# Kernel tuning notes

Measured on AMD Instinct MI355X. Metric: run time of the kernel, lower is better.

The kernel has to match this reference:

```python
import jax, jax.numpy as jnp
import numpy as np

B, K, DIN, D, NH, HD, FF = 16384, 64, 49, 16, 2, 8, 32
EPS = 1e-5


def _ln(x, g, b):
    m = jnp.mean(x, axis=-1, keepdims=True)
    v = jnp.mean((x - m) ** 2, axis=-1, keepdims=True)
    return (x - m) / jnp.sqrt(v + EPS) * g + b


def setup_inputs() -> dict:
    key = jax.random.key(0)
    ks = jax.random.split(key, 20)
    s = 0.05
    return {
        "x": jax.random.normal(ks[0], (B, K, DIN), dtype=jnp.float32),
        # torch Linear layout: weight is [out, in]
        "proj_w": jax.random.normal(ks[1], (D, DIN), dtype=jnp.float32) * s,
        "proj_b": jax.random.normal(ks[2], (D,), dtype=jnp.float32) * s,
        "pos": jax.random.normal(ks[3], (1, K, D), dtype=jnp.float32) * s,
        "in_proj_w": jax.random.normal(ks[4], (3 * D, D), dtype=jnp.float32) * s,
        "in_proj_b": jax.random.normal(ks[5], (3 * D,), dtype=jnp.float32) * s,
        "out_w": jax.random.normal(ks[6], (D, D), dtype=jnp.float32) * s,
        "out_b": jax.random.normal(ks[7], (D,), dtype=jnp.float32) * s,
        "ln1_g": jnp.ones((D,), dtype=jnp.float32),
        "ln1_b": jnp.zeros((D,), dtype=jnp.float32),
        "lin1_w": jax.random.normal(ks[8], (FF, D), dtype=jnp.float32) * s,
        "lin1_b": jax.random.normal(ks[9], (FF,), dtype=jnp.float32) * s,
        "lin2_w": jax.random.normal(ks[10], (D, FF), dtype=jnp.float32) * s,
        "lin2_b": jax.random.normal(ks[11], (D,), dtype=jnp.float32) * s,
        "ln2_g": jnp.ones((D,), dtype=jnp.float32),
        "ln2_b": jnp.zeros((D,), dtype=jnp.float32),
        "head_w": jax.random.normal(ks[12], (1, D), dtype=jnp.float32) * s,
        "head_b": jax.random.normal(ks[13], (1,), dtype=jnp.float32) * s,
    }


def reference(x, proj_w, proj_b, pos, in_proj_w, in_proj_b, out_w, out_b,
              ln1_g, ln1_b, lin1_w, lin1_b, lin2_w, lin2_b, ln2_g, ln2_b,
              head_w, head_b):
    # input projection + learned positional embedding
    h = jnp.einsum("bki,di->bkd", x, proj_w) + proj_b + pos  # [B,K,D]

    # --- self-attention (torch MultiheadAttention, post-norm encoder layer) ---
    qkv = jnp.einsum("bkd,ed->bke", h, in_proj_w) + in_proj_b  # [B,K,3D]
    q, k, v = jnp.split(qkv, 3, axis=-1)
    q = q.reshape(B, K, NH, HD)
    k = k.reshape(B, K, NH, HD)
    v = v.reshape(B, K, NH, HD)
    scores = jnp.einsum("bqhd,bkhd->bhqk", q, k) / jnp.sqrt(jnp.float32(HD))
    attn = jax.nn.softmax(scores, axis=-1)
    ctx = jnp.einsum("bhqk,bkhd->bqhd", attn, v).reshape(B, K, D)
    attn_out = jnp.einsum("bkd,od->bko", ctx, out_w) + out_b
    h = _ln(h + attn_out, ln1_g, ln1_b)

    # --- FFN (relu), post-norm ---
    ff = jnp.einsum("bkd,fd->bkf", h, lin1_w) + lin1_b
    ff = jax.nn.relu(ff)
    ff = jnp.einsum("bkf,df->bkd", ff, lin2_w) + lin2_b
    h = _ln(h + ff, ln2_g, ln2_b)

    # mean pool over sequence, then scalar head
    pooled = h.mean(axis=1)  # [B,D]
    out = jnp.einsum("bd,od->bo", pooled, head_w) + head_b
    return out.squeeze(-1)  # [B]
```

## Files before the change

### kernel.cpp

```cpp
#include <hip/hip_runtime.h>


#define SCALE 0.510069729f

#define KRS   40
#define VTB   2560
#define VTS   72
#define PRB   3712
#define PRS   72
#define HRB   8320
#define HRS   40
#define RED   10880
#define SMTOT 10888

#define WS_HB   2304
#define WS_EP   3328

typedef __bf16 v8bf __attribute__((ext_vector_type(8)));
typedef float  v4f  __attribute__((ext_vector_type(4)));

#define LDS_ORDER() __asm__ volatile("" ::: "memory")

static __device__ __forceinline__ short f2bs(float f) {
    __bf16 h = (__bf16)f;
    return __builtin_bit_cast(short, h);
}
#define MFMA(a,b,c) __builtin_amdgcn_mfma_f32_16x16x32_bf16((a),(b),(c),0,0,0)

template<int IMM> static __device__ __forceinline__ float swz(float x) {
    return __builtin_bit_cast(float,
        __builtin_amdgcn_ds_swizzle(__builtin_bit_cast(int, x), IMM));
}

static __device__ __forceinline__ void red16(v4f& v) {
    #pragma unroll
    for (int r = 0; r < 4; ++r) v[r] += swz<0x041F>(v[r]);
    #pragma unroll
    for (int r = 0; r < 4; ++r) v[r] += swz<0x081F>(v[r]);
    #pragma unroll
    for (int r = 0; r < 4; ++r) v[r] += swz<0x101F>(v[r]);
    #pragma unroll
    for (int r = 0; r < 4; ++r) v[r] += swz<0x201F>(v[r]);
}

__global__ __launch_bounds__(64)
void tx_prep(const float* __restrict__ proj_w, const float* __restrict__ proj_b,
             const float* __restrict__ pos,
             const float* __restrict__ in_proj_w, const float* __restrict__ in_proj_b,
             const float* __restrict__ out_w, const float* __restrict__ out_b,
             const float* __restrict__ ln1_g, const float* __restrict__ ln1_b,
             const float* __restrict__ lin1_w, const float* __restrict__ lin1_b,
             const float* __restrict__ lin2_w, const float* __restrict__ lin2_b,
             const float* __restrict__ ln2_g, const float* __restrict__ ln2_b,
             const float* __restrict__ head_w, float* __restrict__ ws)
{
    const int lane = threadIdx.x, g = lane >> 4, c = lane & 15;
    v8bf* wf = (v8bf*)ws;
    v8bf F;
    #pragma unroll
    for (int j = 0; j < 8; ++j) F[j] = (__bf16)proj_w[c*49 + g*8 + j];
    wf[0*64 + lane] = F;
    #pragma unroll
    for (int j = 0; j < 8; ++j) { int k = 32 + g*8 + j; F[j] = (k < 49) ? (__bf16)proj_w[c*49 + k] : (__bf16)0.f; }
    wf[1*64 + lane] = F;
    #pragma unroll
    for (int nt = 0; nt < 3; ++nt) {
        #pragma unroll
        for (int j = 0; j < 8; ++j) { int k = g*8 + j; F[j] = (k < 16) ? (__bf16)in_proj_w[(nt*16 + c)*16 + k] : (__bf16)0.f; }
        wf[(2 + nt)*64 + lane] = F;
    }
    #pragma unroll
    for (int j = 0; j < 8; ++j) { int k = g*8 + j; F[j] = (k < 16) ? (__bf16)out_w[c*16 + k] : (__bf16)0.f; }
    wf[5*64 + lane] = F;
    #pragma unroll
    for (int nt = 0; nt < 2; ++nt) {
        #pragma unroll
        for (int j = 0; j < 8; ++j) { int k = g*8 + j; F[j] = (k < 16) ? (__bf16)lin1_w[(nt*16 + c)*16 + k] : (__bf16)0.f; }
        wf[(6 + nt)*64 + lane] = F;
    }
    #pragma unroll
    for (int j = 0; j < 8; ++j) F[j] = (__bf16)lin2_w[c*32 + g*8 + j];
    wf[8*64 + lane] = F;

    float* hb = ws + WS_HB;
    #pragma unroll
    for (int ww = 0; ww < 4; ++ww)
        #pragma unroll
        for (int r = 0; r < 4; ++r)
            hb[ww*256 + r*64 + lane] = proj_b[c] + pos[(ww*16 + g*4 + r)*16 + c];

    if (lane < 16) {
        float* ep = ws + WS_EP + lane*16;
        ep[0]  = in_proj_b[lane];
        ep[1]  = in_proj_b[16 + lane] * SCALE;
        ep[2]  = in_proj_b[32 + lane];
        ep[3]  = out_b[lane];
        ep[4]  = ln1_g[lane];
        ep[5]  = ln1_b[lane];
        ep[6]  = lin1_b[lane];
        ep[7]  = lin1_b[16 + lane];
        ep[8]  = lin2_b[lane];
        ep[9]  = ln2_g[lane];
        ep[10] = ln2_b[lane];
        ep[11] = head_w[lane];
        ep[12] = 0.f; ep[13] = 0.f; ep[14] = 0.f; ep[15] = 0.f;
    }
}

__global__ __launch_bounds__(256, 7)
void tx_main(const float* __restrict__ x, const float* __restrict__ ws,
             const float* __restrict__ head_b, float* __restrict__ out)
{
    __shared__ __align__(16) short sm[SMTOT];
    const int tid   = threadIdx.x;
    const int w     = tid >> 6;
    const int lane  = tid & 63;
    const int g     = lane >> 4;
    const int c     = lane & 15;
    const int b     = blockIdx.x;
    const int myrow = w*16 + c;
    const int tok0  = w*16 + g*4;
    const v8bf* wf  = (const v8bf*)ws;
    const float4* ep4 = (const float4*)(ws + WS_EP);
    float* smf = (float*)sm;

    v8bf zfrag;
    #pragma unroll
    for (int j = 0; j < 8; ++j) zfrag[j] = (__bf16)0.f;
    const v4f zacc = {0.f, 0.f, 0.f, 0.f};

    const float4* xb4 = (const float4*)(x + (size_t)b * 3136);
    float4* sf4 = (float4*)smf;
    #pragma unroll
    for (int i = 0; i < 3; ++i) sf4[tid + i*256] = xb4[tid + i*256];
    if (tid < 16)      sf4[768 + tid] = xb4[768 + tid];
    else if (tid < 32) smf[3136 + tid - 16] = 0.f;
    *(unsigned long long*)&sm[HRB + myrow*HRS + 16 + g*4] = 0ull;
    __syncthreads();

    v4f hC;
    {
        const float* xr = smf + myrow*49 + g*8;
        v8bf a0, a1;
        #pragma unroll
        for (int j = 0; j < 8; ++j) a0[j] = (__bf16)xr[j];
        #pragma unroll
        for (int j = 0; j < 8; ++j) a1[j] = (__bf16)xr[32 + j];
        v8bf Bp0 = wf[0*64 + lane], Bp1 = wf[1*64 + lane];
        hC = MFMA(a0, Bp0, zacc);
        hC = MFMA(a1, Bp1, hC);
        const float* hb = ws + WS_HB;
        #pragma unroll
        for (int r = 0; r < 4; ++r) hC[r] += hb[w*256 + r*64 + lane];
        #pragma unroll
        for (int r = 0; r < 4; ++r) sm[HRB + (tok0 + r)*HRS + c] = f2bs(hC[r]);
    }
    __syncthreads();

    {
        v8bf Bq0 = wf[2*64 + lane], Bq1 = wf[3*64 + lane], Bq2 = wf[4*64 + lane];
        v8bf a = *(const v8bf*)&sm[HRB + myrow*HRS + g*8];
        v4f qC = MFMA(a, Bq0, zacc);
        v4f kC = MFMA(a, Bq1, zacc);
        v4f vC = MFMA(a, Bq2, zacc);
        float4 e0 = ep4[c*4];
        #pragma unroll
        for (int r = 0; r < 4; ++r) {
            int tok = tok0 + r;
            sm[HRB + tok*HRS + c] = f2bs(qC[r] + e0.x);
            sm[tok*KRS + c]       = f2bs(fmaf(kC[r], SCALE, e0.y));
            sm[VTB + c*VTS + tok] = f2bs(vC[r] + e0.z);
        }
    }
    __syncthreads();

    v4f ctxC0, ctxC1;
    {
        v8bf aq = *(const v8bf*)&sm[HRB + myrow*HRS + g*8];
        const int ch  = c >> 3;
        const int pwb = PRB + tok0*PRS + (c & 7);
        const int prd = PRB + myrow*PRS + ((g ^ ((myrow >> 2) & 3)) << 3);
        #pragma unroll
        for (int hh = 0; hh < 2; ++hh) {
            v4f sC[4];
            #pragma unroll
            for (int tj = 0; tj < 4; ++tj) {
                v8bf bk = zfrag;
                if (g == hh) bk = *(const v8bf*)&sm[(tj*16 + c)*KRS + g*8];
                sC[tj] = MFMA(aq, bk, zacc);
            }
            #pragma unroll
            for (int tj = 0; tj < 4; ++tj) {
                int po = pwb + (((tj*2 + ch) ^ g) << 3);
                #pragma unroll
                for (int r = 0; r < 4; ++r)
                    sm[po + r*PRS] = f2bs(__builtin_amdgcn_exp2f(sC[tj][r]));
            }
            v8bf bv0 = zfrag, bv1 = zfrag;
            bool act  = (hh == 0) ? (c < 8) : (c >= 8);
            int  onec = (hh == 0) ? 8 : 7;
            if (act) {
                bv0 = *(const v8bf*)&sm[VTB + c*VTS + g*8];
                bv1 = *(const v8bf*)&sm[VTB + c*VTS + 32 + g*8];
            } else if (c == onec) {
                #pragma unroll
                for (int j = 0; j < 8; ++j) { bv0[j] = (__bf16)1.f; bv1[j] = (__bf16)1.f; }
            }
            LDS_ORDER();
            v4f acc = zacc;
            acc = MFMA(*(const v8bf*)&sm[prd],      bv0, acc);
            acc = MFMA(*(const v8bf*)&sm[prd + 32], bv1, acc);
            if (hh) ctxC1 = acc; else ctxC0 = acc;
            LDS_ORDER();
        }
    }

    {
        #pragma unroll
        for (int r = 0; r < 4; ++r) {
            float l0 = swz<0x110>(ctxC0[r]);
            float l1 = swz<0x0F0>(ctxC1[r]);
            float num = (c < 8) ? ctxC0[r] : ctxC1[r];
            float den = (c < 8) ? l0 : l1;
            sm[HRB + (tok0 + r)*HRS + c] = f2bs(num * __builtin_amdgcn_rcpf(den));
        }
    }
    LDS_ORDER();

    v4f hln;
    {
        v8bf Bo = wf[5*64 + lane];
        v8bf a = *(const v8bf*)&sm[HRB + myrow*HRS + g*8];
        v4f oC = MFMA(a, Bo, zacc);
        float4 e0 = ep4[c*4];
        float4 e1 = ep4[c*4 + 1];
        v4f hn;
        #pragma unroll
        for (int r = 0; r < 4; ++r) hn[r] = hC[r] + oC[r] + e0.w;
        v4f s = hn;
        red16(s);
        v4f t, vs;
        #pragma unroll
        for (int r = 0; r < 4; ++r) { t[r] = hn[r] - s[r]*0.0625f; vs[r] = t[r]*t[r]; }
        red16(vs);
        #pragma unroll
        for (int r = 0; r < 4; ++r) {
            float is = __builtin_amdgcn_rsqf(fmaf(vs[r], 0.0625f, 1e-5f));
            hln[r] = t[r]*is*e1.x + e1.y;
            sm[HRB + (tok0 + r)*HRS + c] = f2bs(hln[r]);
        }
    }
    LDS_ORDER();

    v4f o2;
    {
        v8bf Bl10 = wf[6*64 + lane], Bl11 = wf[7*64 + lane], Bl2 = wf[8*64 + lane];
        v8bf a = *(const v8bf*)&sm[HRB + myrow*HRS + g*8];
        v4f f0 = MFMA(a, Bl10, zacc);
        v4f f1 = MFMA(a, Bl11, zacc);
        float4 e1 = ep4[c*4 + 1];
        #pragma unroll
        for (int r = 0; r < 4; ++r) {
            int tok = tok0 + r;
            sm[HRB + tok*HRS + c]      = f2bs(fmaxf(f0[r] + e1.z, 0.f));
            sm[HRB + tok*HRS + 16 + c] = f2bs(fmaxf(f1[r] + e1.w, 0.f));
        }
        LDS_ORDER();
        v8bf a2 = *(const v8bf*)&sm[HRB + myrow*HRS + g*8];
        o2 = MFMA(a2, Bl2, zacc);
    }

    float part = 0.f;
    {
        float4 e2 = ep4[c*4 + 2];
        v4f hn;
        #pragma unroll
        for (int r = 0; r < 4; ++r) hn[r] = hln[r] + o2[r] + e2.x;
        v4f s = hn;
        red16(s);
        v4f t, vs;
        #pragma unroll
        for (int r = 0; r < 4; ++r) { t[r] = hn[r] - s[r]*0.0625f; vs[r] = t[r]*t[r]; }
        red16(vs);
        #pragma unroll
        for (int r = 0; r < 4; ++r) {
            float is = __builtin_amdgcn_rsqf(fmaf(vs[r], 0.0625f, 1e-5f));
            float h3 = t[r]*is*e2.y + e2.z;
            part = fmaf(h3, e2.w, part);
        }
    }
    part += swz<0x041F>(part);
    part += swz<0x081F>(part);
    part += swz<0x101F>(part);
    part += swz<0x201F>(part);
    part += swz<0x401F>(part);
    part += __shfl_xor(part, 32, 64);
    float* fred = (float*)&sm[RED];
    if (lane == 0) fred[w] = part;
    __syncthreads();
    if (tid == 0)
        out[b] = (fred[0] + fred[1] + fred[2] + fred[3]) * (1.f/64.f) + head_b[0];
}

extern "C" void kernel_launch(void* const* d_in, const int* in_sizes, int n_in,
                              void* d_out, int out_size, void* d_ws, size_t ws_size,
                              hipStream_t stream) {
    const float* x         = (const float*)d_in[0];
    const float* proj_w    = (const float*)d_in[1];
    const float* proj_b    = (const float*)d_in[2];
    const float* pos       = (const float*)d_in[3];
    const float* in_proj_w = (const float*)d_in[4];
    const float* in_proj_b = (const float*)d_in[5];
    const float* out_w     = (const float*)d_in[6];
    const float* out_b     = (const float*)d_in[7];
    const float* ln1_g     = (const float*)d_in[8];
    const float* ln1_b     = (const float*)d_in[9];
    const float* lin1_w    = (const float*)d_in[10];
    const float* lin1_b    = (const float*)d_in[11];
    const float* lin2_w    = (const float*)d_in[12];
    const float* lin2_b    = (const float*)d_in[13];
    const float* ln2_g     = (const float*)d_in[14];
    const float* ln2_b     = (const float*)d_in[15];
    const float* head_w    = (const float*)d_in[16];
    const float* head_b    = (const float*)d_in[17];
    float* ws = (float*)d_ws;

    tx_prep<<<1, 64, 0, stream>>>(proj_w, proj_b, pos, in_proj_w, in_proj_b,
                                  out_w, out_b, ln1_g, ln1_b, lin1_w, lin1_b,
                                  lin2_w, lin2_b, ln2_g, ln2_b, head_w, ws);
    tx_main<<<16384, 256, 0, stream>>>(x, ws, head_b, (float*)d_out);
}
```

Before: 336.0 us.

## Shrink K row stride, vectorize bias load, single-pass LayerNorm statistics

Reduces the K-row LDS stride from 40 to 24 shorts and shifts all later LDS regions down, cutting shared memory per block so 8 blocks per CU can fit. The launch-bounds occupancy hint rises from 7 to 8 to match. The precomputed proj-bias+pos table is re-laid out so each lane loads its four values with one vector load instead of four scalar loads. Both LayerNorms now compute sum and sum-of-squares independently, so the two cross-lane reductions no longer depend on each other, at some risk of reduced numerical accuracy from E[x^2]-mean^2.

```diff
diff --git a/kernel.cpp b/kernel.cpp
--- a/kernel.cpp
+++ b/kernel.cpp
@@ -3,15 +3,15 @@
 
 #define SCALE 0.510069729f
 
-#define KRS   40
-#define VTB   2560
+#define KRS   24
+#define VTB   1536
 #define VTS   72
-#define PRB   3712
+#define PRB   2688
 #define PRS   72
-#define HRB   8320
+#define HRB   7296
 #define HRS   40
-#define RED   10880
-#define SMTOT 10888
+#define RED   9856
+#define SMTOT 9864
 
 #define WS_HB   2304
 #define WS_EP   3328
@@ -87,7 +87,7 @@
     for (int ww = 0; ww < 4; ++ww)
         #pragma unroll
         for (int r = 0; r < 4; ++r)
-            hb[ww*256 + r*64 + lane] = proj_b[c] + pos[(ww*16 + g*4 + r)*16 + c];
+            hb[ww*256 + lane*4 + r] = proj_b[c] + pos[(ww*16 + g*4 + r)*16 + c];
 
     if (lane < 16) {
         float* ep = ws + WS_EP + lane*16;
@@ -107,7 +107,7 @@
     }
 }
 
-__global__ __launch_bounds__(256, 7)
+__global__ __launch_bounds__(256, 8)
 void tx_main(const float* __restrict__ x, const float* __restrict__ ws,
              const float* __restrict__ head_b, float* __restrict__ out)
 {
@@ -149,9 +149,9 @@
         v8bf Bp0 = wf[0*64 + lane], Bp1 = wf[1*64 + lane];
         hC = MFMA(a0, Bp0, zacc);
         hC = MFMA(a1, Bp1, hC);
-        const float* hb = ws + WS_HB;
-        #pragma unroll
-        for (int r = 0; r < 4; ++r) hC[r] += hb[w*256 + r*64 + lane];
+        v4f hb = ((const v4f*)(ws + WS_HB))[w*64 + lane];
+        #pragma unroll
+        for (int r = 0; r < 4; ++r) hC[r] += hb[r];
         #pragma unroll
         for (int r = 0; r < 4; ++r) sm[HRB + (tok0 + r)*HRS + c] = f2bs(hC[r]);
     }
@@ -234,19 +234,17 @@
         v4f oC = MFMA(a, Bo, zacc);
         float4 e0 = ep4[c*4];
         float4 e1 = ep4[c*4 + 1];
-        v4f hn;
-        #pragma unroll
-        for (int r = 0; r < 4; ++r) hn[r] = hC[r] + oC[r] + e0.w;
-        v4f s = hn;
+        v4f hn, s, q;
+        #pragma unroll
+        for (int r = 0; r < 4; ++r) { hn[r] = hC[r] + oC[r] + e0.w; s[r] = hn[r]; q[r] = hn[r]*hn[r]; }
         red16(s);
-        v4f t, vs;
-        #pragma unroll
-        for (int r = 0; r < 4; ++r) { t[r] = hn[r] - s[r]*0.0625f; vs[r] = t[r]*t[r]; }
-        red16(vs);
-        #pragma unroll
-        for (int r = 0; r < 4; ++r) {
-            float is = __builtin_amdgcn_rsqf(fmaf(vs[r], 0.0625f, 1e-5f));
-            hln[r] = t[r]*is*e1.x + e1.y;
+        red16(q);
+        #pragma unroll
+        for (int r = 0; r < 4; ++r) {
+            float mean = s[r]*0.0625f;
+            float var  = fmaf(q[r], 0.0625f, -mean*mean);
+            float is = __builtin_amdgcn_rsqf(var + 1e-5f);
+            hln[r] = (hn[r] - mean)*is*e1.x + e1.y;
             sm[HRB + (tok0 + r)*HRS + c] = f2bs(hln[r]);
         }
     }
@@ -273,19 +271,17 @@
     float part = 0.f;
     {
         float4 e2 = ep4[c*4 + 2];
-        v4f hn;
-        #pragma unroll
-        for (int r = 0; r < 4; ++r) hn[r] = hln[r] + o2[r] + e2.x;
-        v4f s = hn;
+        v4f hn, s, q;
+        #pragma unroll
+        for (int r = 0; r < 4; ++r) { hn[r] = hln[r] + o2[r] + e2.x; s[r] = hn[r]; q[r] = hn[r]*hn[r]; }
         red16(s);
-        v4f t, vs;
-        #pragma unroll
-        for (int r = 0; r < 4; ++r) { t[r] = hn[r] - s[r]*0.0625f; vs[r] = t[r]*t[r]; }
-        red16(vs);
-        #pragma unroll
-        for (int r = 0; r < 4; ++r) {
-            float is = __builtin_amdgcn_rsqf(fmaf(vs[r], 0.0625f, 1e-5f));
-            float h3 = t[r]*is*e2.y + e2.z;
+        red16(q);
+        #pragma unroll
+        for (int r = 0; r < 4; ++r) {
+            float mean = s[r]*0.0625f;
+            float var  = fmaf(q[r], 0.0625f, -mean*mean);
+            float is = __builtin_amdgcn_rsqf(var + 1e-5f);
+            float h3 = (hn[r] - mean)*is*e2.y + e2.z;
             part = fmaf(h3, e2.w, part);
         }
     }
```

After: 332.8 us. Within noise of the previous version (-0.9%).
